# Performance work log

Measured on AMD Instinct MI355X. Metric: run time of the kernel, lower is better.

Reference implementation:

```python
import jax, jax.numpy as jnp
import numpy as np

EPS = 1e-12


def _phi(e):
    # e: [C, L] -> pairwise euclidean distances [C, C], diagonal zeroed
    sq = jnp.sum(e * e, axis=1)                      # [C]
    prod = e @ e.T                                   # [C, C]
    d2 = sq[:, None] + sq[None, :] - 2.0 * prod
    d = jnp.sqrt(jnp.clip(d2, EPS, None))
    C = e.shape[0]
    return d * (1.0 - jnp.eye(C, dtype=e.dtype))


def setup_inputs() -> dict:
    key = jax.random.key(0)
    k1, k2, k3 = jax.random.split(key, 3)
    N, C, L = 64, 512, 256
    le_student = jax.random.normal(k1, (N, C, L), dtype=jnp.float32)
    le_teacher = jax.random.normal(k2, (N, C, L), dtype=jnp.float32)
    targets = jax.random.randint(k3, (N, C), 0, 2, dtype=jnp.int32)
    return {"le_student": le_student, "le_teacher": le_teacher, "targets": targets}


def reference(le_student, le_teacher, targets):
    N, C, L = le_student.shape
    m = targets.astype(le_student.dtype)             # [N, C] 0/1 mask
    es = le_student * m[:, :, None]                  # zero out negative rows
    et = le_teacher * m[:, :, None]

    Ds = jax.vmap(_phi)(es)                          # [N, C, C]
    Dt = jax.vmap(_phi)(et)                          # [N, C, C]

    eye = jnp.eye(C, dtype=m.dtype)
    pm = m[:, :, None] * m[:, None, :]               # pairs of positive rows
    offdiag = pm * (1.0 - eye)                       # off-diagonal positive pairs

    npos = jnp.sum(m, axis=1)                        # [N]
    cnt = npos * (npos - 1.0)                        # entries with d > 0 in submatrix
    valid = npos > 1.0
    safe_cnt = jnp.maximum(cnt, 1.0)

    mean_s = jnp.sum(Ds * offdiag, axis=(1, 2)) / safe_cnt
    mean_t = jax.lax.stop_gradient(jnp.sum(Dt * offdiag, axis=(1, 2)) / safe_cnt)
    mean_s = jnp.where(valid, mean_s, 1.0)
    mean_t = jnp.where(valid, mean_t, 1.0)

    d = Ds / mean_s[:, None, None]
    td = jax.lax.stop_gradient(Dt / mean_t[:, None, None])

    diff = d - td
    adiff = jnp.abs(diff)
    huber = jnp.where(adiff < 1.0, 0.5 * diff * diff, adiff - 0.5)

    per = jnp.sum(huber * pm, axis=(1, 2)) / jnp.maximum(npos, 1.0)
    return jnp.sum(jnp.where(valid, per, 0.0))
```

## Files before the change

### kernel.cpp

```cpp
#include <hip/hip_runtime.h>
#include <hip/hip_bf16.h>
#include <hip/hip_fp16.h>
#include <math.h>

#define NB 64
#define CC 512
#define LL 256

typedef __attribute__((ext_vector_type(4))) float floatx4;
typedef __attribute__((ext_vector_type(8))) short short8;

static __device__ __forceinline__ unsigned f2bf2(float x, float y) {
    __hip_bfloat162 h = __float22bfloat162_rn(make_float2(x, y));
    union { __hip_bfloat162 h; unsigned u; } c; c.h = h;
    return c.u;
}
static __device__ __forceinline__ unsigned f2h(float x) {
    __half h = __float2half_rn(x);
    union { __half h; unsigned short u; } c; c.h = h;
    return (unsigned)c.u;
}
static __device__ __forceinline__ float h2f(unsigned u) {
    union { unsigned short u; __half h; } c; c.u = (unsigned short)u;
    return __half2float(c.h);
}

__global__ __launch_bounds__(256) void dist_kernel(
    const float* __restrict__ S, const float* __restrict__ T,
    const int* __restrict__ targets,
    float* __restrict__ psumS, float* __restrict__ psumT,
    int* __restrict__ npos_ws, unsigned* __restrict__ D,
    float* __restrict__ out)
{
    const int lin = blockIdx.x, n = blockIdx.y;
    int tI = 0, rem = lin;
    while (rem >= 8 - tI) { rem -= 8 - tI; ++tI; }
    const int tJ = tI + rem;
    const bool diag = (tI == tJ);

    __shared__ int s_idx[CC];
    __shared__ int s_cnt[8], s_off[8];
    __shared__ int s_npS;
    __shared__ __align__(16) unsigned short lds[4][64][40];
    __shared__ float s_norm[4][64];
    __shared__ float redA[4], redB[4];

    const int tid = threadIdx.x;
    const int w = tid >> 6, lane = tid & 63;

    const int* tg = targets + n * CC;
    const bool p0 = tg[tid] != 0;
    const bool p1 = tg[tid + 256] != 0;
    const unsigned long long m0 = __ballot(p0);
    const unsigned long long m1 = __ballot(p1);
    if (lane == 0) { s_cnt[w] = __popcll(m0); s_cnt[4 + w] = __popcll(m1); }
    __syncthreads();
    if (tid == 0) {
        int a = 0;
        for (int i = 0; i < 8; ++i) { s_off[i] = a; a += s_cnt[i]; }
        s_npS = a;
    }
    __syncthreads();
    const unsigned long long below = (1ull << lane) - 1ull;
    if (p0) s_idx[s_off[w] + __popcll(m0 & below)] = tid;
    if (p1) s_idx[s_off[4 + w] + __popcll(m1 & below)] = tid + 256;
    __syncthreads();
    const int np = s_npS;

    if (tid == 0 && lin == 0) {
        npos_ws[n] = np;
        if (n == 0) out[0] = 0.0f;
    }

    const bool work = (np >= 2) && (tI * 64 < np) && (tJ * 64 < np);

    float t0 = 0.0f, t1 = 0.0f;
    if (work) {
        const bool stager = (!diag) || ((w & 1) == 0);
        const char* Pbase = (const char*)(((w >> 1) ? T : S) + (size_t)n * CC * LL);
        const int tileBase = ((w & 1) ? tJ : tI) * 64;
        const int r8 = lane >> 3, c8 = lane & 7;
        unsigned off_[8];
        #pragma unroll
        for (int i = 0; i < 8; ++i) {
            const int gk = tileBase + r8 + 8 * i;
            const int row = s_idx[(gk < np) ? gk : 0];
            off_[i] = (unsigned)(row * LL * 4 + c8 * 16);
        }

        float4 pre[8];
        float nprt[8];
        #pragma unroll
        for (int i = 0; i < 8; ++i) nprt[i] = 0.0f;
        if (stager) {
            #pragma unroll
            for (int i = 0; i < 8; ++i) pre[i] = *(const float4*)(Pbase + off_[i]);
        }

        const int m16 = lane & 15, quad = lane >> 4;
        const int bufB = diag ? 0 : 1;
        const int wrow = w * 16;

        floatx4 accS[4], accT[4];
        #pragma unroll
        for (int c = 0; c < 4; ++c) {
            accS[c][0] = 0; accS[c][1] = 0; accS[c][2] = 0; accS[c][3] = 0;
            accT[c][0] = 0; accT[c][1] = 0; accT[c][2] = 0; accT[c][3] = 0;
        }

        for (int kk = 0; kk < 8; ++kk) {
            __syncthreads();
            if (stager) {
                #pragma unroll
                for (int i = 0; i < 8; ++i) {
                    nprt[i] += pre[i].x * pre[i].x + pre[i].y * pre[i].y +
                               pre[i].z * pre[i].z + pre[i].w * pre[i].w;
                    *(uint2*)&lds[w][r8 + 8 * i][c8 * 4] =
                        make_uint2(f2bf2(pre[i].x, pre[i].y), f2bf2(pre[i].z, pre[i].w));
                }
            }
            __syncthreads();
            if (stager && kk < 7) {
                #pragma unroll
                for (int i = 0; i < 8; ++i)
                    pre[i] = *(const float4*)(Pbase + off_[i] + (kk + 1) * 128);
            }
            const int aoff = (wrow + m16) * 40 + quad * 8;
            const short8 a_s = *(const short8*)(&lds[0][0][0] + aoff);
            const short8 a_t = *(const short8*)(&lds[2][0][0] + aoff);
            #pragma unroll
            for (int c = 0; c < 4; ++c) {
                const int boff = (c * 16 + m16) * 40 + quad * 8;
                const short8 b_s = *(const short8*)(&lds[bufB][0][0] + boff);
                const short8 b_t = *(const short8*)(&lds[2 + bufB][0][0] + boff);
                accS[c] = __builtin_amdgcn_mfma_f32_16x16x32_bf16(a_s, b_s, accS[c], 0, 0, 0);
                accT[c] = __builtin_amdgcn_mfma_f32_16x16x32_bf16(a_t, b_t, accT[c], 0, 0, 0);
            }
        }

        if (stager) {
            #pragma unroll
            for (int i = 0; i < 8; ++i) {
                float v = nprt[i];
                v += __shfl_xor(v, 1); v += __shfl_xor(v, 2); v += __shfl_xor(v, 4);
                if (c8 == 0) s_norm[w][r8 + 8 * i] = v;
            }
        }
        __syncthreads();

        unsigned* Dn = D + (((size_t)n * 36 + lin) << 12);
        float l0 = 0.0f, l1 = 0.0f;
        #pragma unroll
        for (int c = 0; c < 4; ++c) {
            const int colL = c * 16 + m16;
            const int gj = tJ * 64 + colL;
            const float nBs = s_norm[bufB][colL];
            const float nBt = s_norm[2 + bufB][colL];
            #pragma unroll
            for (int r = 0; r < 4; ++r) {
                const int rowL = wrow + quad * 4 + r;
                const int gi = tI * 64 + rowL;
                const float ds = sqrtf(fmaxf(s_norm[0][rowL] + nBs - 2.0f * accS[c][r], 1e-12f));
                const float dt = sqrtf(fmaxf(s_norm[2][rowL] + nBt - 2.0f * accT[c][r], 1e-12f));
                if (gi < np && gj < np && gi != gj) { l0 += ds; l1 += dt; }
                Dn[rowL * 64 + colL] = f2h(ds) | (f2h(dt) << 16);
            }
        }

        #pragma unroll
        for (int o = 32; o; o >>= 1) { l0 += __shfl_down(l0, o); l1 += __shfl_down(l1, o); }
        if (lane == 0) { redA[w] = l0; redB[w] = l1; }
        __syncthreads();
        if (tid == 0) {
            const float wgt = diag ? 1.0f : 2.0f;
            t0 = wgt * (redA[0] + redA[1] + redA[2] + redA[3]);
            t1 = wgt * (redB[0] + redB[1] + redB[2] + redB[3]);
        }
    }
    if (tid == 0) { psumS[lin * 64 + n] = t0; psumT[lin * 64 + n] = t1; }
}

__global__ __launch_bounds__(256) void huber_kernel(
    const unsigned* __restrict__ D, const int* __restrict__ npos,
    const float* __restrict__ psumS, const float* __restrict__ psumT,
    float* __restrict__ out)
{
    const int lin = blockIdx.x, n = blockIdx.y;
    int tI = 0, rem = lin;
    while (rem >= 8 - tI) { rem -= 8 - tI; ++tI; }
    const int tJ = tI + rem;

    const int np = npos[n];
    if (np < 2) return;
    if (tI * 64 >= np || tJ * 64 >= np) return;

    float ss = 0.0f, st = 0.0f;
    #pragma unroll
    for (int t = 0; t < 36; ++t) { ss += psumS[t * 64 + n]; st += psumT[t * 64 + n]; }
    const float cnt = (float)np * (float)(np - 1);
    const float inv_ms = cnt / ss;
    const float inv_mt = cnt / st;

    const uint4* Dn = (const uint4*)(D + (((size_t)n * 36 + lin) << 12));
    const int tid = threadIdx.x;

    float h = 0.0f;
    #pragma unroll
    for (int it = 0; it < 4; ++it) {
        const int e4 = it * 256 + tid;
        const uint4 v = Dn[e4];
        const unsigned vv[4] = { v.x, v.y, v.z, v.w };
        const int e0 = e4 * 4;
        #pragma unroll
        for (int k = 0; k < 4; ++k) {
            const int e = e0 + k;
            const int gi = tI * 64 + (e >> 6);
            const int gj = tJ * 64 + (e & 63);
            if (gi < np && gj < np && gi != gj) {
                const float ds = h2f(vv[k] & 0xffffu);
                const float dt = h2f(vv[k] >> 16);
                const float diff = ds * inv_ms - dt * inv_mt;
                const float ad = fabsf(diff);
                h += (ad < 1.0f) ? 0.5f * diff * diff : ad - 0.5f;
            }
        }
    }

    #pragma unroll
    for (int o = 32; o; o >>= 1) h += __shfl_down(h, o);
    __shared__ float red[4];
    const int w = tid >> 6, lane = tid & 63;
    if (lane == 0) red[w] = h;
    __syncthreads();
    if (tid == 0) {
        const float wgt = (tI == tJ) ? 1.0f : 2.0f;
        atomicAdd(out, wgt * (red[0] + red[1] + red[2] + red[3]) / (float)np);
    }
}

extern "C" void kernel_launch(void* const* d_in, const int* in_sizes, int n_in,
                              void* d_out, int out_size, void* d_ws, size_t ws_size,
                              hipStream_t stream) {
    const float* S = (const float*)d_in[0];
    const float* T = (const float*)d_in[1];
    const int* targets = (const int*)d_in[2];
    float* out = (float*)d_out;

    float* psumS = (float*)d_ws;
    float* psumT = psumS + 2304;
    int* npos_ws = (int*)(psumT + 2304);
    size_t off = ((size_t)((char*)(npos_ws + 64) - (char*)d_ws) + 255) & ~(size_t)255;
    unsigned* D = (unsigned*)((char*)d_ws + off);

    dim3 grid(36, NB);
    dist_kernel<<<grid, 256, 0, stream>>>(S, T, targets, psumS, psumT, npos_ws, D, out);
    huber_kernel<<<grid, 256, 0, stream>>>(D, npos_ws, psumS, psumT, out);
}
```

Measured before the change: 136.5 us.

## Fuse distance and Huber kernels with per-batch grid spin barrier

Merges the distance kernel and the Huber kernel into one launch. Each block keeps its packed fp16 distances in registers instead of writing the tile to global memory and reading it back. Per-batch distance sums are gathered with atomics, and the blocks of a batch meet at a counter-based spin barrier to get the mean before computing the Huber loss. A small zero kernel clears the accumulators first. This removes a large global intermediate and one launch, but it relies on the blocks of each batch being resident at the same time and adds spin-wait cost.

New measurement: 289.9 us. 112% more time.

```diff
diff --git a/kernel.cpp b/kernel.cpp
--- a/kernel.cpp
+++ b/kernel.cpp
@@ -25,14 +25,21 @@
     return __half2float(c.h);
 }
 
-__global__ __launch_bounds__(256) void dist_kernel(
+__global__ void zero_kernel(float* sumS, float* sumT, int* cnt, float* out) {
+    const int t = threadIdx.x;
+    if (t < NB) { sumS[t] = 0.0f; sumT[t] = 0.0f; }
+    cnt[t] = 0;
+    if (t == 0) out[0] = 0.0f;
+}
+
+__global__ __launch_bounds__(256) void fused_kernel(
     const float* __restrict__ S, const float* __restrict__ T,
     const int* __restrict__ targets,
-    float* __restrict__ psumS, float* __restrict__ psumT,
-    int* __restrict__ npos_ws, unsigned* __restrict__ D,
-    float* __restrict__ out)
+    float* __restrict__ sumS, float* __restrict__ sumT,
+    int* __restrict__ cnt, float* __restrict__ out)
 {
-    const int lin = blockIdx.x, n = blockIdx.y;
+    const int bx = blockIdx.x;
+    const int n = bx / 36, lin = bx - n * 36;
     int tI = 0, rem = lin;
     while (rem >= 8 - tI) { rem -= 8 - tI; ++tI; }
     const int tJ = tI + rem;
@@ -44,6 +51,7 @@
     __shared__ __align__(16) unsigned short lds[4][64][40];
     __shared__ float s_norm[4][64];
     __shared__ float redA[4], redB[4];
+    __shared__ float s_inv[2];
 
     const int tid = threadIdx.x;
     const int w = tid >> 6, lane = tid & 63;
@@ -67,14 +75,14 @@
     __syncthreads();
     const int np = s_npS;
 
-    if (tid == 0 && lin == 0) {
-        npos_ws[n] = np;
-        if (n == 0) out[0] = 0.0f;
-    }
-
     const bool work = (np >= 2) && (tI * 64 < np) && (tJ * 64 < np);
 
+    const int m16 = lane & 15, quad = lane >> 4;
+    const int bufB = diag ? 0 : 1;
+    const int wrow = w * 16;
+    unsigned dpk[16];
     float t0 = 0.0f, t1 = 0.0f;
+
     if (work) {
         const bool stager = (!diag) || ((w & 1) == 0);
         const char* Pbase = (const char*)(((w >> 1) ? T : S) + (size_t)n * CC * LL);
@@ -96,10 +104,6 @@
             #pragma unroll
             for (int i = 0; i < 8; ++i) pre[i] = *(const float4*)(Pbase + off_[i]);
         }
-
-        const int m16 = lane & 15, quad = lane >> 4;
-        const int bufB = diag ? 0 : 1;
-        const int wrow = w * 16;
 
         floatx4 accS[4], accT[4];
         #pragma unroll
@@ -148,7 +152,6 @@
         }
         __syncthreads();
 
-        unsigned* Dn = D + (((size_t)n * 36 + lin) << 12);
         float l0 = 0.0f, l1 = 0.0f;
         #pragma unroll
         for (int c = 0; c < 4; ++c) {
@@ -163,7 +166,7 @@
                 const float ds = sqrtf(fmaxf(s_norm[0][rowL] + nBs - 2.0f * accS[c][r], 1e-12f));
                 const float dt = sqrtf(fmaxf(s_norm[2][rowL] + nBt - 2.0f * accT[c][r], 1e-12f));
                 if (gi < np && gj < np && gi != gj) { l0 += ds; l1 += dt; }
-                Dn[rowL * 64 + colL] = f2h(ds) | (f2h(dt) << 16);
+                dpk[c * 4 + r] = f2h(ds) | (f2h(dt) << 16);
             }
         }
 
@@ -177,65 +180,54 @@
             t1 = wgt * (redB[0] + redB[1] + redB[2] + redB[3]);
         }
     }
-    if (tid == 0) { psumS[lin * 64 + n] = t0; psumT[lin * 64 + n] = t1; }
-}
-
-__global__ __launch_bounds__(256) void huber_kernel(
-    const unsigned* __restrict__ D, const int* __restrict__ npos,
-    const float* __restrict__ psumS, const float* __restrict__ psumT,
-    float* __restrict__ out)
-{
-    const int lin = blockIdx.x, n = blockIdx.y;
-    int tI = 0, rem = lin;
-    while (rem >= 8 - tI) { rem -= 8 - tI; ++tI; }
-    const int tJ = tI + rem;
-
-    const int np = npos[n];
-    if (np < 2) return;
-    if (tI * 64 >= np || tJ * 64 >= np) return;
-
-    float ss = 0.0f, st = 0.0f;
-    #pragma unroll
-    for (int t = 0; t < 36; ++t) { ss += psumS[t * 64 + n]; st += psumT[t * 64 + n]; }
-    const float cnt = (float)np * (float)(np - 1);
-    const float inv_ms = cnt / ss;
-    const float inv_mt = cnt / st;
-
-    const uint4* Dn = (const uint4*)(D + (((size_t)n * 36 + lin) << 12));
-    const int tid = threadIdx.x;
-
+
+    if (tid == 0) {
+        if (work) {
+            if (t0 != 0.0f) atomicAdd(&sumS[n], t0);
+            if (t1 != 0.0f) atomicAdd(&sumT[n], t1);
+        }
+        __threadfence();
+        __hip_atomic_fetch_add(&cnt[n * 16], 1, __ATOMIC_ACQ_REL, __HIP_MEMORY_SCOPE_AGENT);
+        if (work) {
+            while (__hip_atomic_load(&cnt[n * 16], __ATOMIC_ACQUIRE,
+                                     __HIP_MEMORY_SCOPE_AGENT) < 36)
+                __builtin_amdgcn_s_sleep(8);
+            const float ss = __hip_atomic_load(&sumS[n], __ATOMIC_RELAXED,
+                                               __HIP_MEMORY_SCOPE_AGENT);
+            const float st = __hip_atomic_load(&sumT[n], __ATOMIC_RELAXED,
+                                               __HIP_MEMORY_SCOPE_AGENT);
+            const float cp = (float)np * (float)(np - 1);
+            s_inv[0] = cp / ss;
+            s_inv[1] = cp / st;
+        }
+    }
+    if (!work) return;
+    __syncthreads();
+
+    const float inv_ms = s_inv[0], inv_mt = s_inv[1];
     float h = 0.0f;
     #pragma unroll
-    for (int it = 0; it < 4; ++it) {
-        const int e4 = it * 256 + tid;
-        const uint4 v = Dn[e4];
-        const unsigned vv[4] = { v.x, v.y, v.z, v.w };
-        const int e0 = e4 * 4;
-        #pragma unroll
-        for (int k = 0; k < 4; ++k) {
-            const int e = e0 + k;
-            const int gi = tI * 64 + (e >> 6);
-            const int gj = tJ * 64 + (e & 63);
+    for (int c = 0; c < 4; ++c) {
+        const int gj = tJ * 64 + c * 16 + m16;
+        #pragma unroll
+        for (int r = 0; r < 4; ++r) {
+            const int gi = tI * 64 + wrow + quad * 4 + r;
             if (gi < np && gj < np && gi != gj) {
-                const float ds = h2f(vv[k] & 0xffffu);
-                const float dt = h2f(vv[k] >> 16);
+                const unsigned u = dpk[c * 4 + r];
+                const float ds = h2f(u & 0xffffu);
+                const float dt = h2f(u >> 16);
                 const float diff = ds * inv_ms - dt * inv_mt;
                 const float ad = fabsf(diff);
                 h += (ad < 1.0f) ? 0.5f * diff * diff : ad - 0.5f;
             }
         }
     }
-
     #pragma unroll
     for (int o = 32; o; o >>= 1) h += __shfl_down(h, o);
-    __shared__ float red[4];
-    const int w = tid >> 6, lane = tid & 63;
-    if (lane == 0) red[w] = h;
-    __syncthreads();
-    if (tid == 0) {
-        const float wgt = (tI == tJ) ? 1.0f : 2.0f;
-        atomicAdd(out, wgt * (red[0] + red[1] + red[2] + red[3]) / (float)np);
-    }
+    if (lane == 0) redA[w] = h;
+    __syncthreads();
+    if (tid == 0)
+        atomicAdd(out, (diag ? 1.0f : 2.0f) * (redA[0] + redA[1] + redA[2] + redA[3]) / (float)np);
 }
 
 extern "C" void kernel_launch(void* const* d_in, const int* in_sizes, int n_in,
@@ -246,13 +238,10 @@
     const int* targets = (const int*)d_in[2];
     float* out = (float*)d_out;
 
-    float* psumS = (float*)d_ws;
-    float* psumT = psumS + 2304;
-    int* npos_ws = (int*)(psumT + 2304);
-    size_t off = ((size_t)((char*)(npos_ws + 64) - (char*)d_ws) + 255) & ~(size_t)255;
-    unsigned* D = (unsigned*)((char*)d_ws + off);
-
-    dim3 grid(36, NB);
-    dist_kernel<<<grid, 256, 0, stream>>>(S, T, targets, psumS, psumT, npos_ws, D, out);
-    huber_kernel<<<grid, 256, 0, stream>>>(D, npos_ws, psumS, psumT, out);
-}
+    float* sumS = (float*)d_ws;
+    float* sumT = sumS + NB;
+    int* cnt = (int*)(sumT + NB);
+
+    zero_kernel<<<1, 1024, 0, stream>>>(sumS, sumT, cnt, out);
+    fused_kernel<<<NB * 36, 256, 0, stream>>>(S, T, targets, sumS, sumT, cnt, out);
+}
```
